# Performance work log

Hardware: AMD Instinct MI355X
Metric: run time of the kernel (lower is better)

The kernel has to match this reference:

```python
import jax, jax.numpy as jnp
import numpy as np

B = 256
K, S = 6, 4  # kernel size and stride of both locally-connected layers


def _lc2d(x, w, b):
    """Locally-connected 2d conv with unshared per-location weights.
    x: (B, C, H, W); w: (O, C*K*K, Ho, Wo); b: (O, Ho, Wo).
    Patches are extracted once (channel-major, kernel dims fastest) and
    contracted per spatial location.
    """
    p = jax.lax.conv_general_dilated_patches(x, (K, K), (S, S), 'VALID')  # (B, C*K*K, Ho, Wo)
    return jnp.einsum('bphw,ophw->bohw', p, w) + b[None]


def setup_inputs() -> dict:
    key = jax.random.key(0)
    ks = jax.random.split(key, 9)
    s = 0.05  # keep activations well-scaled through the relu stack
    f32 = jnp.float32
    return {
        'x': jax.random.normal(ks[0], (B, 3, 218, 178), f32),
        'w1': jax.random.normal(ks[1], (8, 3 * K * K, 54, 44), f32) * s,
        'b1': jax.random.normal(ks[2], (8, 54, 44), f32) * s,
        'w2': jax.random.normal(ks[3], (16, 8 * K * K, 13, 10), f32) * s,
        'b2': jax.random.normal(ks[4], (16, 13, 10), f32) * s,
        'fc1_w': jax.random.normal(ks[5], (300, 480), f32) * s,
        'fc1_b': jax.random.normal(ks[6], (300,), f32) * s,
        'fc2_w': jax.random.normal(ks[7], (200, 300), f32) * s,
        'fc2_b': jax.random.normal(ks[8], (200,), f32) * s,
    }


def reference(x, w1, b1, w2, b2, fc1_w, fc1_b, fc2_w, fc2_b):
    h = jax.nn.relu(_lc2d(x, w1, b1))           # (B, 8, 54, 44)
    h = jax.nn.relu(_lc2d(h, w2, b2))           # (B, 16, 13, 10)
    # MaxPool2d(2), floor mode: drop the odd trailing row -> (B, 16, 6, 5)
    h = h[:, :, :12, :].reshape(h.shape[0], 16, 6, 2, 5, 2).max(axis=(3, 5))
    h = h.reshape(h.shape[0], -1)               # (B, 480), C-major like torch Flatten
    h = jax.nn.relu(h @ fc1_w.T + fc1_b)        # (B, 300)
    h = h @ fc2_w.T + fc2_b                     # (B, 200)
    return jax.nn.softmax(h, axis=1)
```

## Files before the change

### kernel.cpp

```cpp
#include <hip/hip_runtime.h>
#include <cmath>

namespace {

constexpr int BATCH = 256;
constexpr int C1 = 3, H1 = 218, W1 = 178;
constexpr int IMG1 = C1 * H1 * W1;
constexpr int PLANE1 = H1 * W1;
constexpr int O1 = 8, HO1 = 54, WO1 = 44;
constexpr int HW1 = HO1 * WO1;
constexpr int P1 = C1 * 36;
constexpr int C2 = 8, H2c = 54, W2c = 44;
constexpr int IMG2 = C2 * H2c * W2c;
constexpr int PLANE2 = H2c * W2c;
constexpr int O2 = 16, HO2 = 13, WO2 = 10;
constexpr int HW2 = HO2 * WO2;
constexpr int P2 = C2 * 36;
constexpr int NPOOL = 480;
constexpr int N1 = 300, N2 = 200;

constexpr int THW = 16;
constexpr int NBB = 64;
constexpr int BJ = 4;

__global__ __launch_bounds__(256) void wt2_kernel(const float* __restrict__ w,
                                                  float* __restrict__ wt) {
  const int idx = blockIdx.x * 256 + threadIdx.x;
  if (idx >= P2 * HW2) return;
  float v[O2];
#pragma unroll
  for (int o = 0; o < O2; ++o) v[o] = w[(size_t)o * (P2 * HW2) + idx];
  float4* dst = reinterpret_cast<float4*>(wt + (size_t)idx * O2);
  dst[0] = make_float4(v[0], v[1], v[2], v[3]);
  dst[1] = make_float4(v[4], v[5], v[6], v[7]);
  dst[2] = make_float4(v[8], v[9], v[10], v[11]);
  dst[3] = make_float4(v[12], v[13], v[14], v[15]);
}

__global__ __launch_bounds__(256, 2) void lc1_kernel(const float* __restrict__ x,
                                                     const float* __restrict__ w1,
                                                     const float* __restrict__ b1,
                                                     float* __restrict__ h1) {
  __shared__ float wl[P1 * 128];
  const int t = threadIdx.x;
  const int wave = t >> 6, lane = t & 63;
  const int b2 = lane >> 4, hwl = lane & 15;
  const int hw0 = blockIdx.x * THW;
  const int hw = hw0 + hwl;
  const bool valid = hw < HW1;
  const int hwc = valid ? hw : HW1 - 1;
  const int ho = hwc / WO1, wo = hwc - ho * WO1;
  const int bb = blockIdx.y * NBB + wave * 16 + b2 * BJ;

  for (int i = t; i < 3456; i += 256) {
    const int o = i / 432, r = i - o * 432;
    const int p = r >> 2, q = r & 3;
    int hq = hw0 + q * 4;
    if (hq > HW1 - 4) hq = HW1 - 4;
    const float4 wv =
        *reinterpret_cast<const float4*>(w1 + ((size_t)o * P1 + p) * HW1 + hq);
    const int base = p * 128 + (o >> 1) * 32 + (hq - hw0) * 2 + (o & 1);
    wl[base] = wv.x;
    wl[base + 2] = wv.y;
    wl[base + 4] = wv.z;
    wl[base + 6] = wv.w;
  }

  float acc[BJ][O1];
#pragma unroll
  for (int o = 0; o < O1; ++o) {
    const float bv = b1[o * HW1 + hwc];
#pragma unroll
    for (int j = 0; j < BJ; ++j) acc[j][o] = bv;
  }

  const float* xbase = x + (size_t)bb * IMG1 + (size_t)(ho * 4) * W1 + wo * 4;

  __syncthreads();

  float xA[BJ][6], xB[BJ][6];

#define LC1_LD(K, XV)                                                          \
  do {                                                                         \
    const int c_ = (K) / 6, kh_ = (K) - c_ * 6;                                \
    const int xo_ = c_ * PLANE1 + kh_ * W1;                                    \
    _Pragma("unroll") for (int j = 0; j < BJ; ++j) {                           \
      const float* xr = xbase + (size_t)j * IMG1 + xo_;                        \
      const float2 a0 = *reinterpret_cast<const float2*>(xr);                  \
      const float2 a1 = *reinterpret_cast<const float2*>(xr + 2);              \
      const float2 a2 = *reinterpret_cast<const float2*>(xr + 4);              \
      XV[j][0] = a0.x; XV[j][1] = a0.y; XV[j][2] = a1.x;                       \
      XV[j][3] = a1.y; XV[j][4] = a2.x; XV[j][5] = a2.y;                       \
    }                                                                          \
  } while (0)

#define LC1_FMA(K, XV)                                                         \
  do {                                                                         \
    const float2* wb_ = reinterpret_cast<const float2*>(wl);                   \
    _Pragma("unroll") for (int kw = 0; kw < 6; ++kw) {                         \
      const int p_ = (K) * 6 + kw;                                             \
      const float2 w01 = wb_[p_ * 64 + hwl];                                   \
      const float2 w23 = wb_[p_ * 64 + 16 + hwl];                              \
      const float2 w45 = wb_[p_ * 64 + 32 + hwl];                              \
      const float2 w67 = wb_[p_ * 64 + 48 + hwl];                              \
      _Pragma("unroll") for (int j = 0; j < BJ; ++j) {                         \
        const float xs = XV[j][kw];                                            \
        acc[j][0] = fmaf(xs, w01.x, acc[j][0]);                                \
        acc[j][1] = fmaf(xs, w01.y, acc[j][1]);                                \
        acc[j][2] = fmaf(xs, w23.x, acc[j][2]);                                \
        acc[j][3] = fmaf(xs, w23.y, acc[j][3]);                                \
        acc[j][4] = fmaf(xs, w45.x, acc[j][4]);                                \
        acc[j][5] = fmaf(xs, w45.y, acc[j][5]);                                \
        acc[j][6] = fmaf(xs, w67.x, acc[j][6]);                                \
        acc[j][7] = fmaf(xs, w67.y, acc[j][7]);                                \
      }                                                                        \
    }                                                                          \
  } while (0)

  LC1_LD(0, xA);
#pragma unroll 1
  for (int k = 0; k < 18; k += 2) {
    LC1_LD(k + 1, xB);
    __builtin_amdgcn_sched_barrier(0);
    LC1_FMA(k, xA);
    if (k + 2 < 18) LC1_LD(k + 2, xA);
    __builtin_amdgcn_sched_barrier(0);
    LC1_FMA(k + 1, xB);
  }
#undef LC1_LD
#undef LC1_FMA

  if (valid) {
#pragma unroll
    for (int j = 0; j < BJ; ++j) {
      float* op = h1 + ((size_t)(bb + j) * O1) * HW1 + hw;
#pragma unroll
      for (int o = 0; o < O1; ++o) op[(size_t)o * HW1] = fmaxf(acc[j][o], 0.f);
    }
  }
}

__global__ __launch_bounds__(256) void lc2_kernel(const float* __restrict__ h1,
                                                  const float* __restrict__ w2t,
                                                  const float* __restrict__ b2,
                                                  float* __restrict__ h2) {
  __shared__ float ws[P2 * O2];
  const int hw = blockIdx.x;
  const int lane = threadIdx.x & 63;
  const int og = threadIdx.x >> 6;
  const int b = blockIdx.y * 64 + lane;
  const int ho = hw / WO2, wo = hw - ho * WO2;

  for (int i = threadIdx.x; i < P2 * O2; i += 256) {
    const int p = i >> 4, o = i & 15;
    ws[i] = w2t[((size_t)p * HW2 + hw) * O2 + o];
  }
  __syncthreads();

  float acc[4];
#pragma unroll
  for (int oi = 0; oi < 4; ++oi) acc[oi] = b2[(og * 4 + oi) * HW2 + hw];

  const float* xb = h1 + (size_t)b * IMG2 + (size_t)(ho * 4) * W2c + wo * 4;

#pragma unroll 1
  for (int c = 0; c < C2; ++c) {
    float xv[6][6];
#pragma unroll
    for (int kh = 0; kh < 6; ++kh) {
      const float* xr = xb + c * PLANE2 + kh * W2c;
      const float2 a0 = *reinterpret_cast<const float2*>(xr);
      const float2 a1 = *reinterpret_cast<const float2*>(xr + 2);
      const float2 a2 = *reinterpret_cast<const float2*>(xr + 4);
      xv[kh][0] = a0.x; xv[kh][1] = a0.y;
      xv[kh][2] = a1.x; xv[kh][3] = a1.y;
      xv[kh][4] = a2.x; xv[kh][5] = a2.y;
    }
    __builtin_amdgcn_sched_barrier(0);
#pragma unroll
    for (int kh = 0; kh < 6; ++kh) {
#pragma unroll
      for (int kw = 0; kw < 6; ++kw) {
        const int p = (c * 6 + kh) * 6 + kw;
        const float4 wv = *reinterpret_cast<const float4*>(&ws[p * O2 + og * 4]);
        acc[0] = fmaf(xv[kh][kw], wv.x, acc[0]);
        acc[1] = fmaf(xv[kh][kw], wv.y, acc[1]);
        acc[2] = fmaf(xv[kh][kw], wv.z, acc[2]);
        acc[3] = fmaf(xv[kh][kw], wv.w, acc[3]);
      }
    }
  }

#pragma unroll
  for (int oi = 0; oi < 4; ++oi) {
    h2[((size_t)b * O2 + og * 4 + oi) * HW2 + hw] = fmaxf(acc[oi], 0.f);
  }
}

__global__ __launch_bounds__(512) void head_kernel(const float* __restrict__ h2,
                                                   const float* __restrict__ fc1w,
                                                   const float* __restrict__ fc1b,
                                                   const float* __restrict__ fc2w,
                                                   const float* __restrict__ fc2b,
                                                   float* __restrict__ out) {
  __shared__ __align__(16) float sp[NPOOL];
  __shared__ __align__(16) float sh[N1];
  __shared__ float sl[N2];
  __shared__ float red[2];
  const int b = blockIdx.x;
  const int tid = threadIdx.x;

  if (tid < NPOOL) {
    const int o = tid / 30, r2 = tid - o * 30;
    const int i = r2 / 5, j = r2 - i * 5;
    const float* base = h2 + ((size_t)(b * O2 + o) * HO2 + 2 * i) * WO2 + 2 * j;
    sp[tid] = fmaxf(fmaxf(base[0], base[1]), fmaxf(base[WO2], base[WO2 + 1]));
  }
  __syncthreads();

  const int wv = tid >> 6, ln = tid & 63;
  const float4* sp4 = reinterpret_cast<const float4*>(sp);
  for (int n = wv; n < N1; n += 8) {
    const float4* wr = reinterpret_cast<const float4*>(fc1w + (size_t)n * NPOOL);
    float4 a = wr[ln], p = sp4[ln];
    float s = fmaf(a.x, p.x, fmaf(a.y, p.y, fmaf(a.z, p.z, a.w * p.w)));
    if (ln < 56) {
      float4 a2 = wr[64 + ln], p2 = sp4[64 + ln];
      s = fmaf(a2.x, p2.x, fmaf(a2.y, p2.y, fmaf(a2.z, p2.z, fmaf(a2.w, p2.w, s))));
    }
#pragma unroll
    for (int off = 32; off > 0; off >>= 1) s += __shfl_xor(s, off, 64);
    if (ln == 0) sh[n] = fmaxf(s + fc1b[n], 0.f);
  }
  __syncthreads();

  const float4* sh4 = reinterpret_cast<const float4*>(sh);
  for (int n = wv; n < N2; n += 8) {
    const float4* wr = reinterpret_cast<const float4*>(fc2w + (size_t)n * N1);
    float4 a = wr[ln], p = sh4[ln];
    float s = fmaf(a.x, p.x, fmaf(a.y, p.y, fmaf(a.z, p.z, a.w * p.w)));
    if (ln < 11) {
      float4 a2 = wr[64 + ln], p2 = sh4[64 + ln];
      s = fmaf(a2.x, p2.x, fmaf(a2.y, p2.y, fmaf(a2.z, p2.z, fmaf(a2.w, p2.w, s))));
    }
#pragma unroll
    for (int off = 32; off > 0; off >>= 1) s += __shfl_xor(s, off, 64);
    if (ln == 0) sl[n] = s + fc2b[n];
  }
  __syncthreads();

  if (wv == 0) {
    float m = fmaxf(fmaxf(sl[ln], sl[ln + 64]), sl[ln + 128]);
    if (ln < 8) m = fmaxf(m, sl[192 + ln]);
#pragma unroll
    for (int off = 32; off > 0; off >>= 1) m = fmaxf(m, __shfl_xor(m, off, 64));
    if (ln == 0) red[0] = m;
  }
  __syncthreads();
  const float mx = red[0];
  if (tid < N2) sl[tid] = expf(sl[tid] - mx);
  __syncthreads();
  if (wv == 0) {
    float s = sl[ln] + sl[ln + 64] + sl[ln + 128] + (ln < 8 ? sl[192 + ln] : 0.f);
#pragma unroll
    for (int off = 32; off > 0; off >>= 1) s += __shfl_xor(s, off, 64);
    if (ln == 0) red[1] = s;
  }
  __syncthreads();
  if (tid < N2) out[(size_t)b * N2 + tid] = sl[tid] / red[1];
}

}

extern "C" void kernel_launch(void* const* d_in, const int* in_sizes, int n_in,
                              void* d_out, int out_size, void* d_ws, size_t ws_size,
                              hipStream_t stream) {
  const float* x     = (const float*)d_in[0];
  const float* w1    = (const float*)d_in[1];
  const float* b1    = (const float*)d_in[2];
  const float* w2    = (const float*)d_in[3];
  const float* b2    = (const float*)d_in[4];
  const float* fc1_w = (const float*)d_in[5];
  const float* fc1_b = (const float*)d_in[6];
  const float* fc2_w = (const float*)d_in[7];
  const float* fc2_b = (const float*)d_in[8];
  float* out = (float*)d_out;

  float* ws  = (float*)d_ws;
  float* w2t = ws;
  float* h1  = w2t + (size_t)O2 * P2 * HW2;
  float* h2  = h1 + (size_t)BATCH * O1 * HW1;

  wt2_kernel<<<(P2 * HW2 + 255) / 256, 256, 0, stream>>>(w2, w2t);
  lc1_kernel<<<dim3((HW1 + THW - 1) / THW, BATCH / NBB), 256, 0, stream>>>(x, w1, b1, h1);
  lc2_kernel<<<dim3(HW2, 4), 256, 0, stream>>>(h1, w2t, b2, h2);
  head_kernel<<<BATCH, 512, 0, stream>>>(h2, fc1_w, fc1_b, fc2_w, fc2_b, out);
}
```

Before: 173.2 us.

## Store layer-1 activations batch-innermost so layer-2 reads coalesce across lanes

The intermediate h1 tensor changes from (B, C, H, W) to (C, H, W, B). lc1 now writes one float4 per output channel covering four consecutive batch rows. lc2's lanes, which index batch, now read contiguous addresses instead of addresses strided by a whole image. The aim is to replace uncoalesced gathers in lc2 with coalesced loads, at the cost of lc1 stores now being strided by BATCH across hw lanes.

```diff
diff --git a/kernel.cpp b/kernel.cpp
--- a/kernel.cpp
+++ b/kernel.cpp
@@ -11,8 +11,6 @@
 constexpr int HW1 = HO1 * WO1;
 constexpr int P1 = C1 * 36;
 constexpr int C2 = 8, H2c = 54, W2c = 44;
-constexpr int IMG2 = C2 * H2c * W2c;
-constexpr int PLANE2 = H2c * W2c;
 constexpr int O2 = 16, HO2 = 13, WO2 = 10;
 constexpr int HW2 = HO2 * WO2;
 constexpr int P2 = C2 * 36;
@@ -40,7 +38,7 @@
 __global__ __launch_bounds__(256, 2) void lc1_kernel(const float* __restrict__ x,
                                                      const float* __restrict__ w1,
                                                      const float* __restrict__ b1,
-                                                     float* __restrict__ h1) {
+                                                     float* __restrict__ h1t) {
   __shared__ float wl[P1 * 128];
   const int t = threadIdx.x;
   const int wave = t >> 6, lane = t & 63;
@@ -132,15 +130,15 @@
 
   if (valid) {
 #pragma unroll
-    for (int j = 0; j < BJ; ++j) {
-      float* op = h1 + ((size_t)(bb + j) * O1) * HW1 + hw;
-#pragma unroll
-      for (int o = 0; o < O1; ++o) op[(size_t)o * HW1] = fmaxf(acc[j][o], 0.f);
-    }
-  }
-}
-
-__global__ __launch_bounds__(256) void lc2_kernel(const float* __restrict__ h1,
+    for (int o = 0; o < O1; ++o) {
+      const float4 v = make_float4(fmaxf(acc[0][o], 0.f), fmaxf(acc[1][o], 0.f),
+                                   fmaxf(acc[2][o], 0.f), fmaxf(acc[3][o], 0.f));
+      *reinterpret_cast<float4*>(h1t + ((size_t)o * HW1 + hw) * BATCH + bb) = v;
+    }
+  }
+}
+
+__global__ __launch_bounds__(256) void lc2_kernel(const float* __restrict__ h1t,
                                                   const float* __restrict__ w2t,
                                                   const float* __restrict__ b2,
                                                   float* __restrict__ h2) {
@@ -161,21 +159,16 @@
 #pragma unroll
   for (int oi = 0; oi < 4; ++oi) acc[oi] = b2[(og * 4 + oi) * HW2 + hw];
 
-  const float* xb = h1 + (size_t)b * IMG2 + (size_t)(ho * 4) * W2c + wo * 4;
-
 #pragma unroll 1
   for (int c = 0; c < C2; ++c) {
+    const float* bc =
+        h1t + ((size_t)(c * H2c + ho * 4) * W2c + wo * 4) * BATCH + b;
     float xv[6][6];
 #pragma unroll
-    for (int kh = 0; kh < 6; ++kh) {
-      const float* xr = xb + c * PLANE2 + kh * W2c;
-      const float2 a0 = *reinterpret_cast<const float2*>(xr);
-      const float2 a1 = *reinterpret_cast<const float2*>(xr + 2);
-      const float2 a2 = *reinterpret_cast<const float2*>(xr + 4);
-      xv[kh][0] = a0.x; xv[kh][1] = a0.y;
-      xv[kh][2] = a1.x; xv[kh][3] = a1.y;
-      xv[kh][4] = a2.x; xv[kh][5] = a2.y;
-    }
+    for (int kh = 0; kh < 6; ++kh)
+#pragma unroll
+      for (int kw = 0; kw < 6; ++kw)
+        xv[kh][kw] = bc[(size_t)(kh * W2c + kw) * BATCH];
     __builtin_amdgcn_sched_barrier(0);
 #pragma unroll
     for (int kh = 0; kh < 6; ++kh) {
@@ -288,11 +281,11 @@
 
   float* ws  = (float*)d_ws;
   float* w2t = ws;
-  float* h1  = w2t + (size_t)O2 * P2 * HW2;
-  float* h2  = h1 + (size_t)BATCH * O1 * HW1;
+  float* h1t = w2t + (size_t)O2 * P2 * HW2;
+  float* h2  = h1t + (size_t)BATCH * O1 * HW1;
 
   wt2_kernel<<<(P2 * HW2 + 255) / 256, 256, 0, stream>>>(w2, w2t);
-  lc1_kernel<<<dim3((HW1 + THW - 1) / THW, BATCH / NBB), 256, 0, stream>>>(x, w1, b1, h1);
-  lc2_kernel<<<dim3(HW2, 4), 256, 0, stream>>>(h1, w2t, b2, h2);
+  lc1_kernel<<<dim3((HW1 + THW - 1) / THW, BATCH / NBB), 256, 0, stream>>>(x, w1, b1, h1t);
+  lc2_kernel<<<dim3(HW2, 4), 256, 0, stream>>>(h1t, w2t, b2, h2);
   head_kernel<<<BATCH, 512, 0, stream>>>(h2, fc1_w, fc1_b, fc2_w, fc2_b, out);
 }
```

New measurement: 138.9 us. -19.8%, faster.
